# Kernel tuning notes

Measured on AMD Instinct MI355X. Metric: run time of the kernel, lower is better.

The kernel has to match this reference:

```python
import jax, jax.numpy as jnp
import numpy as np
from jax import lax

H = 2048      # hidden_size
S = 8192      # seq_len (single packed sequence, batch=1)
HK = 8        # num_key_heads
HV = 16       # num_value_heads
DK = 128      # key_head_dim
DV = 128      # value_head_dim
KCONV = 4     # conv kernel size
CHUNK = 64    # chunk size for gated delta rule
EPS = 1e-6    # rms_norm_eps / l2norm eps
CONV_DIM = 2 * HK * DK + HV * DV  # 4096


def setup_inputs() -> dict:
    key = jax.random.key(0)
    ks = jax.random.split(key, 9)
    def w(k, shape, scale):
        return jax.random.normal(k, shape, jnp.float32) * scale
    return {
        "hidden_states": jax.random.normal(ks[0], (1, S, H), jnp.float32),
        "W_qkv": w(ks[1], (H, CONV_DIM), H ** -0.5),
        "W_z": w(ks[2], (H, HV * DV), H ** -0.5),
        "W_b": w(ks[3], (H, HV), H ** -0.5),
        "W_a": w(ks[4], (H, HV), H ** -0.5),
        "conv_w": w(ks[5], (CONV_DIM, KCONV), KCONV ** -0.5),  # depthwise, weight.squeeze(1)
        "A_log": jnp.log(jax.random.uniform(ks[6], (HV,), jnp.float32, 1e-2, 16.0)),
        "dt_bias": jnp.ones((HV,), jnp.float32),
        "norm_w": jnp.ones((DV,), jnp.float32),
        "W_out": w(ks[7], (HV * DV, H), (HV * DV) ** -0.5),
    }


def _l2norm(x):
    return x * lax.rsqrt(jnp.sum(x * x, axis=-1, keepdims=True) + EPS)


def _chunk_gated_delta_rule(q, k, v, g, beta):
    # q,k: [S,Hv,DK]; v: [S,Hv,DV]; g,beta: [S,Hv]. use_qk_l2norm_in_kernel=True.
    scale = DK ** -0.5
    q = _l2norm(q) * scale
    k = _l2norm(k)
    v = v * beta[..., None]
    k_beta = k * beta[..., None]
    n = S // CHUNK
    def chunkify(x):
        return x.reshape(n, CHUNK, HV, x.shape[-1]).transpose(0, 2, 1, 3)  # [n,Hv,C,d]
    q, k, v, k_beta = map(chunkify, (q, k, v, k_beta))
    g = jnp.cumsum(g.reshape(n, CHUNK, HV).transpose(0, 2, 1), axis=-1)  # [n,Hv,C]
    tril_s = jnp.tril(jnp.ones((CHUNK, CHUNK), bool), -1)   # strictly lower
    tril = jnp.tril(jnp.ones((CHUNK, CHUNK), bool))         # incl diagonal
    diff = g[..., :, None] - g[..., None, :]                 # [n,Hv,C,C]
    neg_inf = jnp.float32(-1e30)
    # WY representation: T = (I - A)^{-1}, A strictly lower
    A = -jnp.einsum('nhid,nhjd->nhij', k_beta, k) * jnp.exp(jnp.where(tril_s, diff, neg_inf))
    A = jnp.where(tril_s, A, 0.0)
    T = jnp.linalg.inv(jnp.eye(CHUNK, dtype=A.dtype) - A)    # [n,Hv,C,C]
    w_ = jnp.einsum('nhij,nhjv->nhiv', T, v)                 # "value" in ref
    u_ = jnp.einsum('nhij,nhjk->nhik', T, k_beta * jnp.exp(g)[..., None])  # k_cumdecay
    Aqk = jnp.einsum('nhid,nhjd->nhij', q, k) * jnp.exp(jnp.where(tril, diff, neg_inf))
    g_exp = jnp.exp(g)
    g_last = g[..., -1]

    def step(state, inp):  # state: [Hv,DK,DV]
        q_i, k_i, Aqk_i, w_i, u_i, gexp_i, glast_i, g_i = inp
        v_prime = jnp.einsum('hck,hkv->hcv', u_i, state)
        v_new = w_i - v_prime
        o_inter = jnp.einsum('hck,hkv->hcv', q_i * gexp_i[..., None], state)
        o_i = o_inter + jnp.einsum('hij,hjv->hiv', Aqk_i, v_new)
        k_dec = k_i * jnp.exp(glast_i[:, None] - g_i)[..., None]
        state = state * jnp.exp(glast_i)[:, None, None] + jnp.einsum('hck,hcv->hkv', k_dec, v_new)
        return state, o_i

    state0 = jnp.zeros((HV, DK, DV), q.dtype)
    _, o = lax.scan(step, state0, (q, k, Aqk, w_, u_, g_exp, g_last, g))  # o: [n,Hv,C,DV]
    return o.transpose(0, 2, 1, 3).reshape(S, HV, DV)


def reference(hidden_states, W_qkv, W_z, W_b, W_a, conv_w, A_log, dt_bias, norm_w, W_out):
    x = hidden_states[0]                       # [S,H], batch==1
    mixed = x @ W_qkv                          # [S,CONV_DIM]
    z = (x @ W_z).reshape(S, HV, DV)
    b = x @ W_b                                # [S,HV]
    a = x @ W_a                                # [S,HV]
    # causal depthwise conv1d (padding=K-1, truncate) + silu
    xp = jnp.pad(mixed, ((KCONV - 1, 0), (0, 0)))
    conv = sum(xp[j:j + S] * conv_w[None, :, j] for j in range(KCONV))
    mixed = jax.nn.silu(conv)
    q, k, v = jnp.split(mixed, [HK * DK, 2 * HK * DK], axis=-1)
    q = q.reshape(S, HK, DK)
    k = k.reshape(S, HK, DK)
    v = v.reshape(S, HV, DV)
    beta = jax.nn.sigmoid(b)                   # [S,HV]
    g = -jnp.exp(A_log) * jax.nn.softplus(a + dt_bias)  # [S,HV]
    rep = HV // HK
    q = jnp.repeat(q, rep, axis=1)             # [S,HV,DK]
    k = jnp.repeat(k, rep, axis=1)
    core = _chunk_gated_delta_rule(q, k, v, g, beta)     # [S,HV,DV]
    # gated RMSNorm: rmsnorm(core) * w * silu(z)
    core = core * lax.rsqrt(jnp.mean(core * core, axis=-1, keepdims=True) + EPS)
    core = core * norm_w * jax.nn.silu(z)
    out = core.reshape(S, HV * DV) @ W_out     # [S,H]
    return out[None]                           # [1,S,H]
```

## Files before the change

kernel.cpp:

```cpp
#include <hip/hip_runtime.h>

#define S_LEN 8192
#define HID 2048
#define HKN 8
#define HVN 16
#define DKD 128
#define DVD 128
#define NCHUNK 128
#define CLEN 64
#define NQKV 4096
#define EPSF 1e-6f

typedef unsigned int u32;
typedef unsigned short u16;
typedef __attribute__((ext_vector_type(8))) short s16x8;
typedef __attribute__((ext_vector_type(4))) float f32x4;

__device__ __forceinline__ float bfraw2f(u16 v) { return __uint_as_float(((u32)v) << 16); }
__device__ __forceinline__ u16 f2bf_rne(float f) {
    u32 u = __float_as_uint(f);
    u32 r = u + 0x7fffu + ((u >> 16) & 1u);
    return (u16)(r >> 16);
}
__device__ __forceinline__ void unpack8(uint4 u, float* f) {
    const u32 a[4] = {u.x, u.y, u.z, u.w};
#pragma unroll
    for (int q = 0; q < 4; ++q) {
        f[2*q]   = __uint_as_float(a[q] << 16);
        f[2*q+1] = __uint_as_float(a[q] & 0xffff0000u);
    }
}
__device__ __forceinline__ uint4 pack8(const float* v) {
    uint4 r;
    r.x = (u32)f2bf_rne(v[0]) | ((u32)f2bf_rne(v[1]) << 16);
    r.y = (u32)f2bf_rne(v[2]) | ((u32)f2bf_rne(v[3]) << 16);
    r.z = (u32)f2bf_rne(v[4]) | ((u32)f2bf_rne(v[5]) << 16);
    r.w = (u32)f2bf_rne(v[6]) | ((u32)f2bf_rne(v[7]) << 16);
    return r;
}

__device__ __forceinline__ void gload_lds16(const u16* g, u16* l) {
    __builtin_amdgcn_global_load_lds((const __attribute__((address_space(1))) unsigned int*)g,
                                     (__attribute__((address_space(3))) unsigned int*)l, 16, 0, 0);
}
__device__ __forceinline__ void gload_lds4(const float* g, u16* l) {
    __builtin_amdgcn_global_load_lds((const __attribute__((address_space(1))) unsigned int*)g,
                                     (__attribute__((address_space(3))) unsigned int*)l, 4, 0, 0);
}

__global__ __launch_bounds__(256) void ba_kernel(const float* __restrict__ x,
                                                 const float* __restrict__ Wb,
                                                 const float* __restrict__ Wa,
                                                 const float* __restrict__ A_log,
                                                 const float* __restrict__ dt_bias,
                                                 float* __restrict__ beta,
                                                 float* __restrict__ g) {
    const int t = threadIdx.x;
    const int row = blockIdx.x * 8 + (t >> 5);
    const int c = t & 31;
    const int cc = c & 15;
    const float* W = (c < 16) ? Wb : Wa;
    const float* xr = x + (size_t)row * HID;
    float acc = 0.f;
    for (int k = 0; k < HID; ++k) acc = fmaf(xr[k], W[k * 16 + cc], acc);
    if (c < 16) {
        beta[row * 16 + cc] = 1.f / (1.f + expf(-acc));
    } else {
        float v = acc + dt_bias[cc];
        float sp = (v > 20.f) ? v : log1pf(expf(v));
        g[row * 16 + cc] = -expf(A_log[cc]) * sp;
    }
}

__global__ __launch_bounds__(256) void cvt_x_kernel(const float* __restrict__ x,
                                                    u16* __restrict__ xb) {
    const size_t i8 = ((size_t)blockIdx.x * 256 + threadIdx.x) << 3;
    float4 a = *(const float4*)(x + i8);
    float4 b = *(const float4*)(x + i8 + 4);
    float v[8] = {a.x, a.y, a.z, a.w, b.x, b.y, b.z, b.w};
    *(uint4*)(xb + i8) = pack8(v);
}

__global__ __launch_bounds__(256) void cvt_wT_kernel(const float* __restrict__ W,
                                                     u16* __restrict__ Wt,
                                                     int N, int K) {
    __shared__ u16 T[64 * 72];
    const int t = threadIdx.x;
    const int n0 = blockIdx.x * 64;
    const int k0 = blockIdx.y * 64;
#pragma unroll
    for (int i = 0; i < 4; ++i) {
        int flat = i * 256 + t;
        int kr = flat >> 4, c4 = (flat & 15) << 2;
        float4 v = *(const float4*)(W + (size_t)(k0 + kr) * N + n0 + c4);
        T[(c4 + 0) * 72 + kr] = f2bf_rne(v.x);
        T[(c4 + 1) * 72 + kr] = f2bf_rne(v.y);
        T[(c4 + 2) * 72 + kr] = f2bf_rne(v.z);
        T[(c4 + 3) * 72 + kr] = f2bf_rne(v.w);
    }
    __syncthreads();
#pragma unroll
    for (int i = 0; i < 2; ++i) {
        int flat = i * 256 + t;
        int n = flat >> 3, k8 = (flat & 7) << 3;
        *(uint4*)(Wt + (size_t)(n0 + n) * K + k0 + k8) = *(const uint4*)(T + n * 72 + k8);
    }
}

template <int F32OUT>
__global__ __launch_bounds__(256) void gemm_bt(const u16* __restrict__ A,
                                               const u16* __restrict__ Bt,
                                               void* __restrict__ Cv,
                                               int M, int N, int K) {
    __shared__ __align__(16) u16 As[128 * 64];
    __shared__ __align__(16) u16 Bs[128 * 64];
    const int t = threadIdx.x;
    const int nwg = gridDim.x * gridDim.y;
    int bid = blockIdx.y * gridDim.x + blockIdx.x;
    bid = (bid & 7) * (nwg >> 3) + (bid >> 3);
    const int n0 = (bid % gridDim.x) * 128;
    const int m0 = (bid / gridDim.x) * 128;
    const int w = t >> 6, lane = t & 63;
    const int wm = (w >> 1) * 64, wn = (w & 1) * 64;
    const int ml = lane & 15, kq = lane >> 4;
    f32x4 acc[4][4];
#pragma unroll
    for (int i = 0; i < 4; ++i)
#pragma unroll
        for (int j = 0; j < 4; ++j) acc[i][j] = (f32x4){0.f, 0.f, 0.f, 0.f};

    for (int k0 = 0; k0 < K; k0 += 64) {
#pragma unroll
        for (int r = 0; r < 4; ++r) {
            int flat = r * 256 + t;
            int row = flat >> 3, kc = (flat & 7) << 3;
            gload_lds16(A  + (size_t)(m0 + row) * K + k0 + kc, As + flat * 8);
            gload_lds16(Bt + (size_t)(n0 + row) * K + k0 + kc, Bs + flat * 8);
        }
        __syncthreads();
#pragma unroll
        for (int ks = 0; ks < 2; ++ks) {
            s16x8 af[4], bfr[4];
#pragma unroll
            for (int mt = 0; mt < 4; ++mt)
                af[mt] = *(const s16x8*)(As + (wm + mt * 16 + ml) * 64 + ks * 32 + kq * 8);
#pragma unroll
            for (int nt = 0; nt < 4; ++nt)
                bfr[nt] = *(const s16x8*)(Bs + (wn + nt * 16 + ml) * 64 + ks * 32 + kq * 8);
#pragma unroll
            for (int mt = 0; mt < 4; ++mt)
#pragma unroll
                for (int nt = 0; nt < 4; ++nt)
                    acc[mt][nt] = __builtin_amdgcn_mfma_f32_16x16x32_bf16(af[mt], bfr[nt], acc[mt][nt], 0, 0, 0);
        }
        __syncthreads();
    }
#pragma unroll
    for (int mt = 0; mt < 4; ++mt)
#pragma unroll
        for (int nt = 0; nt < 4; ++nt)
#pragma unroll
            for (int r = 0; r < 4; ++r) {
                int row = m0 + wm + mt * 16 + kq * 4 + r;
                int col = n0 + wn + nt * 16 + ml;
                float v = acc[mt][nt][r];
                if (F32OUT)
                    ((float*)Cv)[(size_t)row * N + col] = v;
                else
                    ((u16*)Cv)[(size_t)row * N + col] = f2bf_rne(v);
            }
}

__global__ __launch_bounds__(512) void prep_kernel(const u16* __restrict__ Cmix,
                                                   const float* __restrict__ conv_w,
                                                   const float* __restrict__ beta,
                                                   u16* __restrict__ qn,
                                                   u16* __restrict__ kn,
                                                   u16* __restrict__ vb) {
    const int s = blockIdx.x;
    const int t = threadIdx.x;
    const int c8 = t << 3;
    __shared__ float ssq[16];
    if (t < 16) ssq[t] = 0.f;

    float y[8];
#pragma unroll
    for (int i = 0; i < 8; ++i) y[i] = 0.f;
    {
        uint4 mrow[4];
#pragma unroll
        for (int j = 0; j < 4; ++j) {
            int r = s - 3 + j;
            if (r >= 0) mrow[j] = *(const uint4*)(Cmix + (size_t)r * NQKV + c8);
            else        mrow[j] = uint4{0u, 0u, 0u, 0u};
        }
        float cw[8][4];
#pragma unroll
        for (int i = 0; i < 8; ++i) {
            float4 cv = *(const float4*)(conv_w + (size_t)(c8 + i) * 4);
            cw[i][0] = cv.x; cw[i][1] = cv.y; cw[i][2] = cv.z; cw[i][3] = cv.w;
        }
#pragma unroll
        for (int j = 0; j < 4; ++j) {
            float mf[8];
            unpack8(mrow[j], mf);
#pragma unroll
            for (int i = 0; i < 8; ++i) y[i] = fmaf(mf[i], cw[i][j], y[i]);
        }
#pragma unroll
        for (int i = 0; i < 8; ++i) {
            float v = y[i];
            y[i] = v / (1.f + expf(-v));
        }
    }
    __syncthreads();
    if (t < 256) {
        float p = 0.f;
#pragma unroll
        for (int i = 0; i < 8; ++i) p += y[i] * y[i];
        atomicAdd(&ssq[t >> 4], p);
    }
    __syncthreads();
    if (t < 128) {
        float rn = rsqrtf(ssq[t >> 4] + EPSF) * 0.08838834764831845f;
        float ov[8];
#pragma unroll
        for (int i = 0; i < 8; ++i) ov[i] = y[i] * rn;
        *(uint4*)(qn + (size_t)s * 1024 + c8) = pack8(ov);
    } else if (t < 256) {
        float rn = rsqrtf(ssq[t >> 4] + EPSF);
        float ov[8];
#pragma unroll
        for (int i = 0; i < 8; ++i) ov[i] = y[i] * rn;
        *(uint4*)(kn + (size_t)s * 1024 + (c8 - 1024)) = pack8(ov);
    } else {
        int vh = (c8 - 2048) >> 7;
        float bb = beta[s * 16 + vh];
        float ov[8];
#pragma unroll
        for (int i = 0; i < 8; ++i) ov[i] = y[i] * bb;
        *(uint4*)(vb + (size_t)s * 2048 + (c8 - 2048)) = pack8(ov);
    }
}

__global__ __launch_bounds__(256, 2) void precomp_kernel(const u16* __restrict__ qn,
                                                         const u16* __restrict__ kn,
                                                         const u16* __restrict__ vb,
                                                         const float* __restrict__ g,
                                                         const float* __restrict__ beta,
                                                         u16* __restrict__ bufB,
                                                         u16* __restrict__ bufK,
                                                         float* __restrict__ egc_arr,
                                                         float* __restrict__ ekd_arr,
                                                         float* __restrict__ eg) {
    const int b = blockIdx.x;
    const int n = b >> 4, h = b & 15, hs = h >> 1;
    const int t = threadIdx.x;
    const int s0 = n * 64;
    u16* BB = bufB + (size_t)b * 20480;

    __shared__ __align__(16) u16 sK[64 * 128];
    __shared__ __align__(16) u16 sVQ[64 * 128];
    __shared__ __align__(16) u16 sKT[64 * 128];
    __shared__ __align__(16) float Am[64 * 64];
    __shared__ float gc[64], bet[64], bexp[64];

    const int w = t >> 6, l = t & 63;
    const int l15 = l & 15, l4 = l >> 4;

#pragma unroll
    for (int i = 0; i < 4; ++i) {
        int flat = i * 256 + t;
        int c = flat >> 4, dc = (flat & 15) << 3;
        int sw = c * 128 + ((((dc >> 3) ^ (c & 7))) << 3);
        *(uint4*)(sK + sw)  = *(const uint4*)(kn + (size_t)(s0 + c) * 1024 + hs * 128 + dc);
        *(uint4*)(sVQ + sw) = *(const uint4*)(vb + (size_t)(s0 + c) * 2048 + h * 128 + dc);
    }
    if (t < 64) {
        gc[t] = g[(size_t)(s0 + t) * 16 + h];
        bet[t] = beta[(size_t)(s0 + t) * 16 + h];
    }
    __syncthreads();
    if (t == 0) {
        float run = 0.f;
        for (int c = 0; c < 64; ++c) { run += gc[c]; gc[c] = run; }
    }
    __syncthreads();
    if (t < 64) {
        float e = expf(gc[t]);
        float ek = expf(gc[63] - gc[t]);
        bexp[t] = bet[t] * e;
        egc_arr[b * 64 + t] = e;
        ekd_arr[b * 64 + t] = ek;
    }
    if (t == 0) eg[b] = expf(gc[63]);
    __syncthreads();

    {
        s16x8 ak[4];
#pragma unroll
        for (int kk = 0; kk < 4; ++kk)
            ak[kk] = *(const s16x8*)(sK + (w * 16 + l15) * 128 + (((kk * 4 + l4) ^ (l15 & 7)) << 3));
        for (int nt = 0; nt <= w; ++nt) {
            f32x4 acc = (f32x4){0.f, 0.f, 0.f, 0.f};
#pragma unroll
            for (int kk = 0; kk < 4; ++kk) {
                s16x8 bk = *(const s16x8*)(sK + (nt * 16 + l15) * 128 + (((kk * 4 + l4) ^ (l15 & 7)) << 3));
                acc = __builtin_amdgcn_mfma_f32_16x16x32_bf16(ak[kk], bk, acc, 0, 0, 0);
            }
            const int j = nt * 16 + l15;
#pragma unroll
            for (int r = 0; r < 4; ++r) {
                int i = w * 16 + l4 * 4 + r;
                if (j < i) Am[i * 64 + j] = -acc[r] * bet[i] * expf(gc[i] - gc[j]);
            }
        }
    }
    uint4 vreg[4];
    {
        const int c = t & 63, db = t >> 6;
#pragma unroll
        for (int r = 0; r < 4; ++r) {
            uint4 kv = *(const uint4*)(sK + c * 128 + ((((4 * db + r) ^ (c & 7))) << 3));
            const u16* kp = (const u16*)&kv;
#pragma unroll
            for (int e = 0; e < 8; ++e) {
                int d = (4 * db + r) * 8 + e;
                sKT[d * 64 + ((((c >> 3) ^ (d & 7))) << 3) + (c & 7)] = kp[e];
            }
            vreg[r] = *(const uint4*)(sVQ + c * 128 + ((((4 * db + r) ^ (c & 7))) << 3));
        }
    }
    __syncthreads();

    {
        const int c = t & 63, db = t >> 6;
#pragma unroll
        for (int r = 0; r < 4; ++r) {
            const u16* vp = (const u16*)&vreg[r];
#pragma unroll
            for (int e = 0; e < 8; ++e) {
                int d = (4 * db + r) * 8 + e;
                sVQ[d * 64 + ((((c >> 3) ^ (d & 7))) << 3) + (c & 7)] = vp[e];
            }
        }
    }
    __syncthreads();

    if (t < 64) {
        float Tc[64];
#pragma unroll
        for (int i = 0; i < 64; ++i) {
            float val = (t == i) ? 1.f : 0.f;
#pragma unroll
            for (int j = 0; j < i; ++j) val = fmaf(Am[i * 64 + j], Tc[j], val);
            Tc[i] = val;
            Am[i * 64 + t] = val;
        }
    }
    __syncthreads();

    float tv[16];
    {
        const int c = t >> 2, j0 = (t & 3) << 4;
#pragma unroll
        for (int q = 0; q < 16; ++q) tv[q] = Am[c * 64 + j0 + q];
    }
    {
        u16* KB = bufK + (size_t)((n << 3) + hs) * 16384;
#pragma unroll
        for (int i = 0; i < 4; ++i) {
            int f = t * 4 + i;
            int d = f >> 3, sb = f & 7;
            uint4 v = *(const uint4*)(sKT + d * 64 + sb * 8);
            if ((h & 1) == 0) *(uint4*)(KB + 8192 + d * 64 + sb * 8) = v;
            int jb = ((sb ^ (d & 7)) << 3);
            float vf[8]; unpack8(v, vf);
#pragma unroll
            for (int e = 0; e < 8; ++e) vf[e] *= bexp[jb + e];
            *(uint4*)(sKT + d * 64 + sb * 8) = pack8(vf);
        }
    }
    __syncthreads();

    {
        u16* Tb = (u16*)Am;
        const int c = t >> 2, j0 = (t & 3) << 4;
        uint4 p0 = pack8(tv), p1 = pack8(tv + 8);
        *(uint4*)(Tb + c * 64 + ((((j0 >> 3) ^ (c & 7))) << 3)) = p0;
        *(uint4*)(Tb + c * 64 + (((((j0 >> 3) + 1) ^ (c & 7))) << 3)) = p1;
    }
    __syncthreads();

    {
        const u16* Tb = (const u16*)Am;
#pragma unroll
        for (int fr2 = 0; fr2 < 2; ++fr2) {
            const int d = w * 32 + fr2 * 16 + l15;
            s16x8 au[2];
#pragma unroll
            for (int kk = 0; kk < 2; ++kk)
                au[kk] = *(const s16x8*)(sKT + d * 64 + (((kk * 4 + l4) ^ (d & 7)) << 3));
#pragma unroll
            for (int fc = 0; fc < 4; ++fc) {
                const int c = fc * 16 + l15;
                f32x4 acc = (f32x4){0.f, 0.f, 0.f, 0.f};
#pragma unroll
                for (int kk = 0; kk < 2; ++kk) {
                    s16x8 bt = *(const s16x8*)(Tb + c * 64 + (((kk * 4 + l4) ^ (c & 7)) << 3));
                    acc = __builtin_amdgcn_mfma_f32_16x16x32_bf16(au[kk], bt, acc, 0, 0, 0);
                }
                const int d0 = w * 32 + fr2 * 16 + l4 * 4;
                uint2 pr;
                pr.x = (u32)f2bf_rne(-acc[0]) | ((u32)f2bf_rne(-acc[1]) << 16);
                pr.y = (u32)f2bf_rne(-acc[2]) | ((u32)f2bf_rne(-acc[3]) << 16);
                *(uint2*)(BB + 8192 + c * 128 + (((d0 >> 3) ^ (c & 7)) << 3) + (d0 & 7)) = pr;
            }
        }
#pragma unroll
        for (int fc2 = 0; fc2 < 2; ++fc2) {
            const int dv = w * 32 + fc2 * 16 + l15;
            s16x8 bv[2];
#pragma unroll
            for (int kk = 0; kk < 2; ++kk)
                bv[kk] = *(const s16x8*)(sVQ + dv * 64 + (((kk * 4 + l4) ^ (dv & 7)) << 3));
#pragma unroll
            for (int fr = 0; fr < 4; ++fr) {
                const int c = fr * 16 + l15;
                f32x4 acc = (f32x4){0.f, 0.f, 0.f, 0.f};
#pragma unroll
                for (int kk = 0; kk < 2; ++kk) {
                    s16x8 at = *(const s16x8*)(Tb + c * 64 + (((kk * 4 + l4) ^ (c & 7)) << 3));
                    acc = __builtin_amdgcn_mfma_f32_16x16x32_bf16(at, bv[kk], acc, 0, 0, 0);
                }
                const int c0 = fr * 16 + l4 * 4;
                uint2 pr;
                pr.x = (u32)f2bf_rne(acc[0]) | ((u32)f2bf_rne(acc[1]) << 16);
                pr.y = (u32)f2bf_rne(acc[2]) | ((u32)f2bf_rne(acc[3]) << 16);
                *(uint2*)(BB + dv * 64 + c0) = pr;
            }
        }
    }
    __syncthreads();

#pragma unroll
    for (int i = 0; i < 4; ++i) {
        int flat = i * 256 + t;
        int c = flat >> 4, dc = (flat & 15) << 3;
        *(uint4*)(sKT + c * 128 + ((((dc >> 3) ^ (c & 7))) << 3)) =
            *(const uint4*)(qn + (size_t)(s0 + c) * 1024 + hs * 128 + dc);
    }
    __syncthreads();

    {
        const u16* sQ = sKT;
        s16x8 aq[4];
#pragma unroll
        for (int kk = 0; kk < 4; ++kk)
            aq[kk] = *(const s16x8*)(sQ + (w * 16 + l15) * 128 + (((kk * 4 + l4) ^ (l15 & 7)) << 3));
#pragma unroll
        for (int nt = 0; nt < 4; ++nt) {
            f32x4 acc = (f32x4){0.f, 0.f, 0.f, 0.f};
            if (nt <= w) {
#pragma unroll
                for (int kk = 0; kk < 4; ++kk) {
                    s16x8 bk = *(const s16x8*)(sK + (nt * 16 + l15) * 128 + (((kk * 4 + l4) ^ (l15 & 7)) << 3));
                    acc = __builtin_amdgcn_mfma_f32_16x16x32_bf16(aq[kk], bk, acc, 0, 0, 0);
                }
            }
            const int jj = nt * 16 + l15;
#pragma unroll
            for (int r = 0; r < 4; ++r) {
                const int i = w * 16 + l4 * 4 + r;
                float val = 0.f;
                if (nt < w || (nt == w && jj <= i)) val = acc[r] * expf(gc[i] - gc[jj]);
                BB[16384 + i * 64 + (((jj >> 3) ^ (i & 7)) << 3) + (jj & 7)] = f2bf_rne(val);
            }
        }
        if ((h & 1) == 0) {
            u16* KB = bufK + (size_t)((n << 3) + hs) * 16384;
#pragma unroll
            for (int i = 0; i < 4; ++i) {
                int f = i * 256 + t;
                int c = f >> 4, sb = f & 15;
                *(uint4*)(KB + c * 128 + sb * 8) = *(const uint4*)(sQ + c * 128 + sb * 8);
            }
        }
    }
}

#define STGA 16512

__global__ __launch_bounds__(256, 1) void scan_state_kernel(const u16* __restrict__ bufB,
                                                            const u16* __restrict__ bufK,
                                                            const float* __restrict__ ekd_g,
                                                            const float* __restrict__ eg_g,
                                                            u16* __restrict__ sstore) {
    __shared__ __align__(16) u16 sStage[2 * STGA];
    __shared__ __align__(16) u16 sSTb[4][16 * 136];
    __shared__ __align__(16) u16 sVTs[4][16 * 72];

    const int h = blockIdx.x >> 1;
    const int dvh = (blockIdx.x & 1) << 6;
    const int hs = h >> 1;
    const int w = threadIdx.x >> 6;
    const int l = threadIdx.x & 63;
    const int l15 = l & 15, l4 = l >> 4, l7 = l & 7;
    const int dv0 = dvh + (w << 4);

    u16* STb = sSTb[w];
    u16* VTs = sVTs[w];

    for (int i = l; i < 16 * 136; i += 64) STb[i] = 0;

    f32x4 Sreg[8];
#pragma unroll
    for (int i = 0; i < 8; ++i) Sreg[i] = (f32x4){0.f, 0.f, 0.f, 0.f};

    auto stage = [&](int n2, u16* dst) {
        const int b2 = (n2 << 4) + h;
        const u16* sU = bufB + (size_t)b2 * 20480 + 8192 + w * 2048 + l * 8;
        u16* dU = dst + w * 2048;
#pragma unroll
        for (int i = 0; i < 4; ++i) gload_lds16(sU + i * 512, dU + i * 512);
        const u16* sKa = bufK + (size_t)((n2 << 3) + hs) * 16384 + 8192 + w * 2048 + l * 8;
        u16* dK = dst + 8192 + w * 2048;
#pragma unroll
        for (int i = 0; i < 4; ++i) gload_lds16(sKa + i * 512, dK + i * 512);
        if (w == 0) gload_lds4(ekd_g + (b2 << 6) + l, dst + 16384);
    };
    auto loadW = [&](int n2, uint2 (&wr)[4]) {
        const u16* wb = bufB + (size_t)((n2 << 4) + h) * 20480 + (size_t)(dv0 + l15) * 64 + l4 * 4;
#pragma unroll
        for (int mt = 0; mt < 4; ++mt) wr[mt] = *(const uint2*)(wb + mt * 16);
    };

    uint2 wA[4], wB[4];
    float egA, egB;
    stage(0, sStage);
    loadW(0, wA);
    egA = eg_g[h];
    __syncthreads();

    int cur = 0;
    for (int n = 0; n < NCHUNK; ++n) {
        const u16* buf = sStage + cur * STGA;
        if (n + 1 < NCHUNK) {
            stage(n + 1, sStage + (cur ^ 1) * STGA);
            loadW(n + 1, wB);
            egB = eg_g[((n + 1) << 4) + h];
        }
        if (n > 0) {
            u16* dstg = sstore + ((size_t)(n * 16 + h)) * 16384 + (size_t)dv0 * 128;
#pragma unroll
            for (int i = 0; i < 4; ++i) {
                int idx = l * 4 + i;
                int row = idx >> 4, col = (idx & 15) << 3;
                *(uint4*)(dstg + row * 128 + col) = *(const uint4*)(STb + row * 136 + col);
            }
        }
        const u16* bU = buf;
        const u16* bK = buf + 8192;
        const float* ekd = (const float*)(buf + 16384);

        s16x8 bF[4];
#pragma unroll
        for (int kk = 0; kk < 4; ++kk)
            bF[kk] = *(const s16x8*)(STb + l15 * 136 + kk * 32 + l4 * 8);

        f32x4 V[4];
#pragma unroll
        for (int mt = 0; mt < 4; ++mt) {
            V[mt][0] = bfraw2f((u16)(wA[mt].x & 0xffffu));
            V[mt][1] = bfraw2f((u16)(wA[mt].x >> 16));
            V[mt][2] = bfraw2f((u16)(wA[mt].y & 0xffffu));
            V[mt][3] = bfraw2f((u16)(wA[mt].y >> 16));
        }
#pragma unroll
        for (int kk = 0; kk < 4; ++kk) {
            const int sw = ((kk * 4 + l4) ^ l7) << 3;
#pragma unroll
            for (int mt = 0; mt < 4; ++mt) {
                s16x8 a = *(const s16x8*)(bU + (mt * 16 + l15) * 128 + sw);
                V[mt] = __builtin_amdgcn_mfma_f32_16x16x32_bf16(a, bF[kk], V[mt], 0, 0, 0);
            }
        }

#pragma unroll
        for (int mt = 0; mt < 4; ++mt) {
            const int cb = mt * 16 + l4 * 4;
            uint2 us;
            us.x = (u32)f2bf_rne(V[mt][0] * ekd[cb]) | ((u32)f2bf_rne(V[mt][1] * ekd[cb + 1]) << 16);
            us.y = (u32)f2bf_rne(V[mt][2] * ekd[cb + 2]) | ((u32)f2bf_rne(V[mt][3] * ekd[cb + 3]) << 16);
            *(uint2*)(VTs + l15 * 72 + cb) = us;
        }

        s16x8 sF0 = *(const s16x8*)(VTs + l15 * 72 + l4 * 8);
        s16x8 sF1 = *(const s16x8*)(VTs + l15 * 72 + 32 + l4 * 8);
#pragma unroll
        for (int nt = 0; nt < 8; ++nt) {
#pragma unroll
            for (int r = 0; r < 4; ++r) Sreg[nt][r] *= egA;
            s16x8 a0 = *(const s16x8*)(bK + (nt * 16 + l15) * 64 + ((l4 ^ l7) << 3));
            Sreg[nt] = __builtin_amdgcn_mfma_f32_16x16x32_bf16(a0, sF0, Sreg[nt], 0, 0, 0);
            s16x8 a1 = *(const s16x8*)(bK + (nt * 16 + l15) * 64 + (((4 + l4) ^ l7) << 3));
            Sreg[nt] = __builtin_amdgcn_mfma_f32_16x16x32_bf16(a1, sF1, Sreg[nt], 0, 0, 0);
        }
#pragma unroll
        for (int nt = 0; nt < 8; ++nt) {
            uint2 sv;
            sv.x = (u32)f2bf_rne(Sreg[nt][0]) | ((u32)f2bf_rne(Sreg[nt][1]) << 16);
            sv.y = (u32)f2bf_rne(Sreg[nt][2]) | ((u32)f2bf_rne(Sreg[nt][3]) << 16);
            *(uint2*)(STb + l15 * 136 + nt * 16 + l4 * 4) = sv;
        }
        __syncthreads();
#pragma unroll
        for (int i = 0; i < 4; ++i) wA[i] = wB[i];
        egA = egB;
        cur ^= 1;
    }
}

__global__ __launch_bounds__(512, 4) void scan_out_kernel(const u16* __restrict__ bufB,
                                                          const u16* __restrict__ bufK,
                                                          const u16* __restrict__ sstore,
                                                          const float* __restrict__ egc_g,
                                                          u16* __restrict__ o) {
    __shared__ __align__(16) u16 sStage[20608];
    __shared__ __align__(16) u16 sVT[8][16 * 72];

    const int bb = blockIdx.x;
    const int n = bb >> 4, h = bb & 15, hs = h >> 1;
    const int t = threadIdx.x;
    const int w = t >> 6, l = t & 63;
    const int l15 = l & 15, l4 = l >> 4, l7 = l & 7;
    const int dv0 = w << 4;
    u16* VT = sVT[w];

#pragma unroll
    for (int i = 0; i < 5; ++i) {
        int c = w + i * 8;
        if (c < 24)
            gload_lds16(bufB + (size_t)bb * 20480 + 8192 + c * 512 + l * 8, sStage + c * 512);
        else
            gload_lds16(bufK + (size_t)((n << 3) + hs) * 16384 + (c - 24) * 512 + l * 8,
                        sStage + 12288 + (c - 24) * 512);
    }
    if (w == 0) gload_lds4(egc_g + (bb << 6) + l, sStage + 20480);

    uint2 wr[4];
    {
        const u16* wb = bufB + (size_t)bb * 20480 + (size_t)(dv0 + l15) * 64 + l4 * 4;
#pragma unroll
        for (int mt = 0; mt < 4; ++mt) wr[mt] = *(const uint2*)(wb + mt * 16);
    }
    s16x8 bF[4];
    if (n > 0) {
        const u16* sp = sstore + (size_t)bb * 16384 + (size_t)(dv0 + l15) * 128 + l4 * 8;
#pragma unroll
        for (int kk = 0; kk < 4; ++kk)
            bF[kk] = *(const s16x8*)(sp + kk * 32);
    }
    __syncthreads();

    const u16* bU = sStage;
    const u16* bA = sStage + 8192;
    const u16* qA = sStage + 12288;
    const float* egc = (const float*)(sStage + 20480);

    f32x4 V[4];
#pragma unroll
    for (int mt = 0; mt < 4; ++mt) {
        V[mt][0] = bfraw2f((u16)(wr[mt].x & 0xffffu));
        V[mt][1] = bfraw2f((u16)(wr[mt].x >> 16));
        V[mt][2] = bfraw2f((u16)(wr[mt].y & 0xffffu));
        V[mt][3] = bfraw2f((u16)(wr[mt].y >> 16));
    }
    f32x4 O[4];
#pragma unroll
    for (int mt = 0; mt < 4; ++mt) O[mt] = (f32x4){0.f, 0.f, 0.f, 0.f};
    if (n > 0) {
#pragma unroll
        for (int kk = 0; kk < 4; ++kk) {
            const int sw = ((kk * 4 + l4) ^ l7) << 3;
#pragma unroll
            for (int mt = 0; mt < 4; ++mt) {
                s16x8 a = *(const s16x8*)(bU + (mt * 16 + l15) * 128 + sw);
                V[mt] = __builtin_amdgcn_mfma_f32_16x16x32_bf16(a, bF[kk], V[mt], 0, 0, 0);
            }
        }
#pragma unroll
        for (int kk = 0; kk < 4; ++kk) {
            const int sw = ((kk * 4 + l4) ^ l7) << 3;
#pragma unroll
            for (int mt = 0; mt < 4; ++mt) {
                s16x8 a = *(const s16x8*)(qA + (mt * 16 + l15) * 128 + sw);
                O[mt] = __builtin_amdgcn_mfma_f32_16x16x32_bf16(a, bF[kk], O[mt], 0, 0, 0);
            }
        }
#pragma unroll
        for (int mt = 0; mt < 4; ++mt)
#pragma unroll
            for (int r = 0; r < 4; ++r) O[mt][r] *= egc[mt * 16 + l4 * 4 + r];
    }

#pragma unroll
    for (int mt = 0; mt < 4; ++mt) {
        const int cb = mt * 16 + l4 * 4;
        uint2 uv;
        uv.x = (u32)f2bf_rne(V[mt][0]) | ((u32)f2bf_rne(V[mt][1]) << 16);
        uv.y = (u32)f2bf_rne(V[mt][2]) | ((u32)f2bf_rne(V[mt][3]) << 16);
        *(uint2*)(VT + l15 * 72 + cb) = uv;
    }
    s16x8 vF0 = *(const s16x8*)(VT + l15 * 72 + l4 * 8);
    s16x8 vF1 = *(const s16x8*)(VT + l15 * 72 + 32 + l4 * 8);
#pragma unroll
    for (int mt = 0; mt < 4; ++mt) {
        s16x8 a = *(const s16x8*)(bA + (mt * 16 + l15) * 64 + ((l4 ^ l7) << 3));
        O[mt] = __builtin_amdgcn_mfma_f32_16x16x32_bf16(a, vF0, O[mt], 0, 0, 0);
    }
#pragma unroll
    for (int mt = 0; mt < 4; ++mt) {
        s16x8 a = *(const s16x8*)(bA + (mt * 16 + l15) * 64 + (((4 + l4) ^ l7) << 3));
        O[mt] = __builtin_amdgcn_mfma_f32_16x16x32_bf16(a, vF1, O[mt], 0, 0, 0);
    }

    const int s0 = n << 6;
#pragma unroll
    for (int mt = 0; mt < 4; ++mt)
#pragma unroll
        for (int r = 0; r < 4; ++r)
            o[(size_t)(s0 + mt * 16 + l4 * 4 + r) * 2048 + (h << 7) + dv0 + l15] = f2bf_rne(O[mt][r]);
}

__global__ __launch_bounds__(256) void gate_kernel(const u16* __restrict__ o,
                                                   const u16* __restrict__ Cz,
                                                   const float* __restrict__ norm_w,
                                                   u16* __restrict__ gated) {
    const int s = blockIdx.x, t = threadIdx.x;
    const int c8 = t << 3, hh = t >> 4;
    __shared__ float ssq[16];
    if (t < 16) ssq[t] = 0.f;
    float ov[8];
    unpack8(*(const uint4*)(o + (size_t)s * 2048 + c8), ov);
    float p = 0.f;
#pragma unroll
    for (int i = 0; i < 8; ++i) p += ov[i] * ov[i];
    __syncthreads();
    atomicAdd(&ssq[hh], p);
    __syncthreads();
    const float rms = rsqrtf(ssq[hh] * 0.0078125f + EPSF);
    float zf[8];
    unpack8(*(const uint4*)(Cz + (size_t)s * 2048 + c8), zf);
    const int d0 = c8 & 127;
    float res[8];
#pragma unroll
    for (int i = 0; i < 8; ++i) {
        float z = zf[i];
        float sz = z / (1.f + expf(-z));
        res[i] = ov[i] * rms * norm_w[d0 + i] * sz;
    }
    *(uint4*)(gated + (size_t)s * 2048 + c8) = pack8(res);
}

extern "C" void kernel_launch(void* const* d_in, const int* in_sizes, int n_in,
                              void* d_out, int out_size, void* d_ws, size_t ws_size,
                              hipStream_t stream) {
    (void)in_sizes; (void)n_in; (void)out_size; (void)ws_size;
    const float* x       = (const float*)d_in[0];
    const float* W_qkv   = (const float*)d_in[1];
    const float* W_z     = (const float*)d_in[2];
    const float* W_b     = (const float*)d_in[3];
    const float* W_a     = (const float*)d_in[4];
    const float* conv_w  = (const float*)d_in[5];
    const float* A_log   = (const float*)d_in[6];
    const float* dt_bias = (const float*)d_in[7];
    const float* norm_w  = (const float*)d_in[8];
    const float* W_out   = (const float*)d_in[9];

    char* p = (char*)d_ws;
    auto alloc = [&](size_t bytes) {
        char* r = p;
        p += (bytes + 255) & ~(size_t)255;
        return r;
    };
    u16* Cmix    = (u16*)alloc((size_t)S_LEN * NQKV * 2);
    char* extra  = alloc((size_t)50331648); (void)extra;
    u16* qn      = (u16*)alloc((size_t)S_LEN * HKN * DKD * 2);
    u16* kn      = (u16*)alloc((size_t)S_LEN * HKN * DKD * 2);
    u16* vb      = (u16*)alloc((size_t)S_LEN * HVN * DVD * 2);
    float* egc   = (float*)alloc((size_t)NCHUNK * HVN * CLEN * 4);
    float* ekd   = (float*)alloc((size_t)NCHUNK * HVN * CLEN * 4);
    float* eg    = (float*)alloc((size_t)NCHUNK * HVN * 4);
    float* beta  = (float*)alloc((size_t)S_LEN * HVN * 4);
    float* g     = (float*)alloc((size_t)S_LEN * HVN * 4);
    u16* bufB  = Cmix;
    u16* bufK  = (u16*)((char*)Cmix + (size_t)83886080);
    u16* o_buf = qn;
    u16* Cz    = vb;
    u16* gated = Cmix;
    u16* xbf    = (u16*)d_out;
    u16* Wq_t   = (u16*)d_out + (size_t)16777216;
    u16* Wz_t   = (u16*)d_out + (size_t)25165824;
    u16* sstore = (u16*)d_out;
    u16* Wout_t = qn;

    ba_kernel<<<S_LEN / 8, 256, 0, stream>>>(x, W_b, W_a, A_log, dt_bias, beta, g);
    cvt_x_kernel<<<S_LEN * HID / (256 * 8), 256, 0, stream>>>(x, xbf);
    cvt_wT_kernel<<<dim3(NQKV / 64, HID / 64), 256, 0, stream>>>(W_qkv, Wq_t, NQKV, HID);
    cvt_wT_kernel<<<dim3(HID / 64, HID / 64), 256, 0, stream>>>(W_z, Wz_t, HID, HID);
    gemm_bt<0><<<dim3(NQKV / 128, S_LEN / 128), 256, 0, stream>>>(xbf, Wq_t, Cmix, S_LEN, NQKV, HID);
    prep_kernel<<<S_LEN, 512, 0, stream>>>(Cmix, conv_w, beta, qn, kn, vb);
    precomp_kernel<<<NCHUNK * HVN, 256, 0, stream>>>(qn, kn, vb, g, beta, bufB, bufK, egc, ekd, eg);
    gemm_bt<0><<<dim3(HID / 128, S_LEN / 128), 256, 0, stream>>>(xbf, Wz_t, Cz, S_LEN, HID, HID);
    scan_state_kernel<<<HVN * 2, 256, 0, stream>>>(bufB, bufK, ekd, eg, sstore);
    scan_out_kernel<<<NCHUNK * HVN, 512, 0, stream>>>(bufB, bufK, sstore, egc, o_buf);
    gate_kernel<<<S_LEN, 256, 0, stream>>>(o_buf, Cz, norm_w, gated);
    cvt_wT_kernel<<<dim3(HID / 64, HID / 64), 256, 0, stream>>>(W_out, Wout_t, HID, HID);
    gemm_bt<1><<<dim3(HID / 128, S_LEN / 128), 256, 0, stream>>>(gated, Wout_t, d_out, S_LEN, HID, HID);
}
```

Before: 1.227 ms.

## Triple-buffer scan_state staging with vmcnt waits and packed bf16 converts

Turns the serial state-scan kernel's double-buffered LDS staging into a three-slot ring that prefetches two chunks ahead. The full __syncthreads is replaced by explicit s_waitcnt vmcnt counts plus a raw barrier, so loads for later chunks can stay in flight while the current one is computed. It also replaces the manual round-to-nearest bf16 conversion with the hardware v_cvt_pk_bf16_f32 instruction. This uses more LDS and relies on hand-counted vmcnt values, which can become wrong if the compiler reorders or splits loads. The final iterations re-stage the last chunk redundantly.

```diff
diff --git a/kernel.cpp b/kernel.cpp
--- a/kernel.cpp
+++ b/kernel.cpp
@@ -21,6 +21,11 @@
     u32 u = __float_as_uint(f);
     u32 r = u + 0x7fffu + ((u >> 16) & 1u);
     return (u16)(r >> 16);
+}
+__device__ __forceinline__ u32 pk_bf16(float lo, float hi) {
+    u32 r;
+    asm("v_cvt_pk_bf16_f32 %0, %1, %2" : "=v"(r) : "v"(lo), "v"(hi));
+    return r;
 }
 __device__ __forceinline__ void unpack8(uint4 u, float* f) {
     const u32 a[4] = {u.x, u.y, u.z, u.w};
@@ -496,7 +501,7 @@
                                                             const float* __restrict__ ekd_g,
                                                             const float* __restrict__ eg_g,
                                                             u16* __restrict__ sstore) {
-    __shared__ __align__(16) u16 sStage[2 * STGA];
+    __shared__ __align__(16) u16 sStage[3 * STGA];
     __shared__ __align__(16) u16 sSTb[4][16 * 136];
     __shared__ __align__(16) u16 sVTs[4][16 * 72];
 
@@ -517,7 +522,8 @@
 #pragma unroll
     for (int i = 0; i < 8; ++i) Sreg[i] = (f32x4){0.f, 0.f, 0.f, 0.f};
 
-    auto stage = [&](int n2, u16* dst) {
+    auto stage = [&](int n2, int slot) {
+        u16* dst = sStage + slot * STGA;
         const int b2 = (n2 << 4) + h;
         const u16* sU = bufB + (size_t)b2 * 20480 + 8192 + w * 2048 + l * 8;
         u16* dU = dst + w * 2048;
@@ -537,19 +543,22 @@
 
     uint2 wA[4], wB[4];
     float egA, egB;
-    stage(0, sStage);
+    stage(0, 0);
+    stage(1, 1);
     loadW(0, wA);
+    loadW(1, wB);
     egA = eg_g[h];
-    __syncthreads();
-
-    int cur = 0;
+    egB = eg_g[16 + h];
+    asm volatile("s_waitcnt vmcnt(16)" ::: "memory");
+    __builtin_amdgcn_s_barrier();
+    asm volatile("" ::: "memory");
+
     for (int n = 0; n < NCHUNK; ++n) {
-        const u16* buf = sStage + cur * STGA;
-        if (n + 1 < NCHUNK) {
-            stage(n + 1, sStage + (cur ^ 1) * STGA);
-            loadW(n + 1, wB);
-            egB = eg_g[((n + 1) << 4) + h];
-        }
+        const u16* buf = sStage + (n % 3) * STGA;
+        asm volatile("s_waitcnt vmcnt(20)" ::: "memory");
+        __builtin_amdgcn_s_barrier();
+        asm volatile("" ::: "memory");
+
         if (n > 0) {
             u16* dstg = sstore + ((size_t)(n * 16 + h)) * 16384 + (size_t)dv0 * 128;
 #pragma unroll
@@ -559,6 +568,18 @@
                 *(uint4*)(dstg + row * 128 + col) = *(const uint4*)(STb + row * 136 + col);
             }
         }
+        {
+            int n2 = (n + 2 < NCHUNK) ? n + 2 : NCHUNK - 1;
+            stage(n2, (n + 2) % 3);
+        }
+        uint2 wC[4];
+        float egC;
+        {
+            int n2 = (n + 2 < NCHUNK) ? n + 2 : NCHUNK - 1;
+            loadW(n2, wC);
+            egC = eg_g[(n2 << 4) + h];
+        }
+
         const u16* bU = buf;
         const u16* bK = buf + 8192;
         const float* ekd = (const float*)(buf + 16384);
@@ -590,8 +611,8 @@
         for (int mt = 0; mt < 4; ++mt) {
             const int cb = mt * 16 + l4 * 4;
             uint2 us;
-            us.x = (u32)f2bf_rne(V[mt][0] * ekd[cb]) | ((u32)f2bf_rne(V[mt][1] * ekd[cb + 1]) << 16);
-            us.y = (u32)f2bf_rne(V[mt][2] * ekd[cb + 2]) | ((u32)f2bf_rne(V[mt][3] * ekd[cb + 3]) << 16);
+            us.x = pk_bf16(V[mt][0] * ekd[cb], V[mt][1] * ekd[cb + 1]);
+            us.y = pk_bf16(V[mt][2] * ekd[cb + 2], V[mt][3] * ekd[cb + 3]);
             *(uint2*)(VTs + l15 * 72 + cb) = us;
         }
 
@@ -609,15 +630,14 @@
 #pragma unroll
         for (int nt = 0; nt < 8; ++nt) {
             uint2 sv;
-            sv.x = (u32)f2bf_rne(Sreg[nt][0]) | ((u32)f2bf_rne(Sreg[nt][1]) << 16);
-            sv.y = (u32)f2bf_rne(Sreg[nt][2]) | ((u32)f2bf_rne(Sreg[nt][3]) << 16);
+            sv.x = pk_bf16(Sreg[nt][0], Sreg[nt][1]);
+            sv.y = pk_bf16(Sreg[nt][2], Sreg[nt][3]);
             *(uint2*)(STb + l15 * 136 + nt * 16 + l4 * 4) = sv;
         }
-        __syncthreads();
-#pragma unroll
-        for (int i = 0; i < 4; ++i) wA[i] = wB[i];
+#pragma unroll
+        for (int i = 0; i < 4; ++i) { wA[i] = wB[i]; wB[i] = wC[i]; }
         egA = egB;
-        cur ^= 1;
+        egB = egC;
     }
 }
 
```

Result: no change. 1.225 ms (-0.2%).
